# Kernel optimization log

Measured on AMD Instinct MI355X. Metric: run time of the kernel, lower is better.

Reference implementation:

```python
import jax, jax.numpy as jnp
import numpy as np

D = 1024        # model dim
H = 8           # num heads
HD = D // H     # head dim = 128
EPS = 1e-6
B, L = 2, 4096


def _rmsnorm(x, g):
    # RMSNorm over the full model dim (applied before head split, as in source)
    return x * jax.lax.rsqrt(jnp.mean(x * x, axis=-1, keepdims=True) + EPS) * g


def _rope_interleaved(x, cos, sin):
    # x: [B, L, H, HD]; cos/sin: [L, HD//2]
    x1 = x[..., 0::2]
    x2 = x[..., 1::2]
    c = cos[None, :, None, :]
    s = sin[None, :, None, :]
    # interleave (x1*c - x2*s, x1*s + x2*c) back into even/odd lanes
    out = jnp.stack([x1 * c - x2 * s, x1 * s + x2 * c], axis=-1)
    return out.reshape(x.shape)


def setup_inputs() -> dict:
    key = jax.random.key(0)
    ks = jax.random.split(key, 6)
    x = jax.random.normal(ks[0], (B, L, D), dtype=jnp.float32)
    freqs_cos = jax.random.uniform(ks[1], (L, HD // 2), dtype=jnp.float32)
    freqs_sin = jax.random.uniform(ks[2], (L, HD // 2), dtype=jnp.float32)
    s = 1.0 / np.sqrt(D).astype(np.float32)
    w_qkv = jax.random.normal(ks[3], (D, 3 * D), dtype=jnp.float32) * s
    b_qkv = jnp.zeros((3 * D,), dtype=jnp.float32)
    g_q = jnp.ones((D,), dtype=jnp.float32)
    g_k = jnp.ones((D,), dtype=jnp.float32)
    w_out = jax.random.normal(ks[4], (D, D), dtype=jnp.float32) * s
    b_out = jnp.zeros((D,), dtype=jnp.float32)
    return {"x": x, "freqs_cos": freqs_cos, "freqs_sin": freqs_sin,
            "w_qkv": w_qkv, "b_qkv": b_qkv, "g_q": g_q, "g_k": g_k,
            "w_out": w_out, "b_out": b_out}


def reference(x, freqs_cos, freqs_sin, w_qkv, b_qkv, g_q, g_k, w_out, b_out):
    Bx, Lx, _ = x.shape
    qkv = x @ w_qkv + b_qkv                      # [B, L, 3D]
    q, k, v = jnp.split(qkv, 3, axis=-1)          # each [B, L, D]
    q = _rmsnorm(q, g_q)
    k = _rmsnorm(k, g_k)
    q = q.reshape(Bx, Lx, H, HD)
    k = k.reshape(Bx, Lx, H, HD)
    v = v.reshape(Bx, Lx, H, HD)
    q = _rope_interleaved(q, freqs_cos, freqs_sin)
    k = _rope_interleaved(k, freqs_cos, freqs_sin)
    scale = 1.0 / np.sqrt(HD)
    scores = jnp.einsum('blhd,bmhd->bhlm', q, k) * scale
    attn = jax.nn.softmax(scores, axis=-1)
    o = jnp.einsum('bhlm,bmhd->blhd', attn, v).reshape(Bx, Lx, D)
    return o @ w_out + b_out
```

## Files before the change

kernel.cpp:

```cpp
#include <hip/hip_runtime.h>
#include <hip/hip_bf16.h>
#include <stdint.h>

typedef __attribute__((ext_vector_type(8))) short short8;
typedef __attribute__((ext_vector_type(4))) short short4v;
typedef __attribute__((ext_vector_type(4))) float f32x4;

#define LSEQ 4096
#define DMODEL 1024
#define NHEAD 8
#define HDIM 128
#define MTOT 8192
#define NQKV 3072

__device__ __forceinline__ unsigned short f2bf(float f){
  unsigned u = __float_as_uint(f);
  u += 0x7fffu + ((u >> 16) & 1u);
  return (unsigned short)(u >> 16);
}
__device__ __forceinline__ float bf2f(unsigned short h){
  return __uint_as_float(((unsigned)h) << 16);
}

typedef const __attribute__((address_space(1))) void* gas_ptr;
typedef __attribute__((address_space(3))) void* las_ptr;
__device__ __forceinline__ void gload_lds16(const void* g, void* l){
  __builtin_amdgcn_global_load_lds((gas_ptr)(uintptr_t)g,
                                   (las_ptr)(unsigned)(uintptr_t)l, 16, 0, 0);
}

__global__ __launch_bounds__(256) void k_cvt(const float* __restrict__ in,
                                             unsigned short* __restrict__ out, int n8){
  int i = blockIdx.x*256 + threadIdx.x;
  if (i >= n8) return;
  const float4* p = (const float4*)in + (size_t)i*2;
  float4 a = p[0], b = p[1];
  short8 r;
  r[0]=(short)f2bf(a.x); r[1]=(short)f2bf(a.y); r[2]=(short)f2bf(a.z); r[3]=(short)f2bf(a.w);
  r[4]=(short)f2bf(b.x); r[5]=(short)f2bf(b.y); r[6]=(short)f2bf(b.z); r[7]=(short)f2bf(b.w);
  *(short8*)(out + (size_t)i*8) = r;
}

__global__ __launch_bounds__(256) void k_transpose_cvt(const float* __restrict__ in,
                                                       unsigned short* __restrict__ out,
                                                       int R, int C){
  __shared__ unsigned short tile[32][33];
  int c0 = blockIdx.x*32, r0 = blockIdx.y*32;
  int tx = threadIdx.x & 31, ty = threadIdx.x >> 5;
  #pragma unroll
  for (int i=0;i<32;i+=8)
    tile[ty+i][tx] = f2bf(in[(size_t)(r0+ty+i)*C + c0+tx]);
  __syncthreads();
  #pragma unroll
  for (int i=0;i<32;i+=8)
    out[(size_t)(c0+ty+i)*R + r0+tx] = tile[tx][ty+i];
}

__global__ __launch_bounds__(256) void k_vT(const unsigned short* __restrict__ qkv,
                                            unsigned short* __restrict__ vT){
  __shared__ unsigned short tile[32][33];
  int bh = blockIdx.z; int b = bh >> 3, h = bh & 7;
  int l0 = blockIdx.x*32, d0 = blockIdx.y*32;
  const unsigned short* src = qkv + (size_t)b*LSEQ*NQKV + 2*DMODEL + h*HDIM;
  int tx = threadIdx.x & 31, ty = threadIdx.x >> 5;
  #pragma unroll
  for (int i=0;i<32;i+=8)
    tile[ty+i][tx] = src[(size_t)(l0+ty+i)*NQKV + d0+tx];
  __syncthreads();
  unsigned short* dst = vT + ((size_t)bh*HDIM + d0)*LSEQ + l0;
  #pragma unroll
  for (int i=0;i<32;i+=8)
    dst[(size_t)(ty+i)*LSEQ + tx] = tile[tx][ty+i];
}

template<int OUT_BF16>
__global__ __launch_bounds__(256) void k_gemm_bt(const unsigned short* __restrict__ A,
                                                 const unsigned short* __restrict__ Bt,
                                                 const float* __restrict__ bias,
                                                 void* __restrict__ Cout,
                                                 int M, int N, int K){
  __shared__ unsigned short As[128*64];
  __shared__ unsigned short Bs[128*64];
  int tid = threadIdx.x, lane = tid & 63, wave = tid >> 6;
  int wm = wave >> 1, wn = wave & 1;
  int m0 = blockIdx.y*128, n0 = blockIdx.x*128;
  f32x4 zero = {0.f,0.f,0.f,0.f};
  f32x4 acc[4][4];
  #pragma unroll
  for (int mi=0;mi<4;++mi)
    #pragma unroll
    for (int ni=0;ni<4;++ni) acc[mi][ni] = zero;

  int srow = lane >> 3;
  int soffb = (lane & 7) * 16;
  int scol = (soffb ^ (srow << 4)) >> 1;
  int cg = lane >> 4, cl = lane & 15;

  int nkt = K >> 6;
  for (int kt = 0; kt < nkt; ++kt){
    if (kt) __syncthreads();
    int kbase = kt*64;
    #pragma unroll
    for (int j=0;j<4;++j){
      int ch = wave*4 + j;
      int row = ch*8 + srow;
      gload_lds16(A  + (size_t)(m0+row)*K + kbase + scol, (char*)As + ch*1024);
      gload_lds16(Bt + (size_t)(n0+row)*K + kbase + scol, (char*)Bs + ch*1024);
    }
    __syncthreads();

    short8 af[4][2], bf[4][2];
    #pragma unroll
    for (int mi=0;mi<4;++mi){
      int row = wm*64 + mi*16 + cl;
      int key = (row & 7) << 4;
      #pragma unroll
      for (int kk=0;kk<2;++kk)
        af[mi][kk] = *(const short8*)((const char*)As + row*128 + ((kk*64 + cg*16) ^ key));
    }
    #pragma unroll
    for (int ni=0;ni<4;++ni){
      int row = wn*64 + ni*16 + cl;
      int key = (row & 7) << 4;
      #pragma unroll
      for (int kk=0;kk<2;++kk)
        bf[ni][kk] = *(const short8*)((const char*)Bs + row*128 + ((kk*64 + cg*16) ^ key));
    }
    #pragma unroll
    for (int kk=0;kk<2;++kk)
      #pragma unroll
      for (int mi=0;mi<4;++mi)
        #pragma unroll
        for (int ni=0;ni<4;++ni)
          acc[mi][ni] = __builtin_amdgcn_mfma_f32_16x16x32_bf16(af[mi][kk], bf[ni][kk], acc[mi][ni], 0,0,0);
  }

  #pragma unroll
  for (int ni=0;ni<4;++ni){
    int col = n0 + wn*64 + ni*16 + cl;
    float bv = bias[col];
    #pragma unroll
    for (int mi=0;mi<4;++mi){
      int r = m0 + wm*64 + mi*16 + cg*4;
      #pragma unroll
      for (int i=0;i<4;++i){
        float v = acc[mi][ni][i] + bv;
        if (OUT_BF16) ((unsigned short*)Cout)[(size_t)(r+i)*N + col] = f2bf(v);
        else          ((float*)Cout)[(size_t)(r+i)*N + col] = v;
      }
    }
  }
}

__global__ __launch_bounds__(256) void k_norm_rope(unsigned short* __restrict__ qkv,
                                                   const float* __restrict__ fcos,
                                                   const float* __restrict__ fsin,
                                                   const float* __restrict__ gq,
                                                   const float* __restrict__ gk){
  int bl = blockIdx.x;
  int l = bl & (LSEQ-1);
  int t = threadIdx.x;
  unsigned short* row = qkv + (size_t)bl * NQKV;
  int d0 = t*4;
  short4v qv = *(short4v*)(row + d0);
  short4v kv = *(short4v*)(row + DMODEL + d0);
  float q[4], k[4];
  #pragma unroll
  for (int j=0;j<4;++j){ q[j] = bf2f((unsigned short)qv[j]); k[j] = bf2f((unsigned short)kv[j]); }
  float sq = q[0]*q[0]+q[1]*q[1]+q[2]*q[2]+q[3]*q[3];
  float sk = k[0]*k[0]+k[1]*k[1]+k[2]*k[2]+k[3]*k[3];
  #pragma unroll
  for (int o=32;o;o>>=1){ sq += __shfl_xor(sq,o); sk += __shfl_xor(sk,o); }
  __shared__ float red[8];
  int lane = t & 63, wv = t >> 6;
  if (!lane){ red[wv] = sq; red[4+wv] = sk; }
  __syncthreads();
  sq = red[0]+red[1]+red[2]+red[3];
  sk = red[4]+red[5]+red[6]+red[7];
  float rq = rsqrtf(sq*(1.f/1024.f) + 1e-6f);
  float rk = rsqrtf(sk*(1.f/1024.f) + 1e-6f);
  int hd = d0 & (HDIM-1);
  int fi = (l << 6) + (hd >> 1);
  float c0 = fcos[fi], s0 = fsin[fi], c1 = fcos[fi+1], s1 = fsin[fi+1];
  {
    float x1 = q[0]*rq*gq[d0],   x2 = q[1]*rq*gq[d0+1];
    float x3 = q[2]*rq*gq[d0+2], x4 = q[3]*rq*gq[d0+3];
    short4v qo;
    qo[0]=(short)f2bf(x1*c0 - x2*s0); qo[1]=(short)f2bf(x1*s0 + x2*c0);
    qo[2]=(short)f2bf(x3*c1 - x4*s1); qo[3]=(short)f2bf(x3*s1 + x4*c1);
    *(short4v*)(row + d0) = qo;
  }
  {
    float x1 = k[0]*rk*gk[d0],   x2 = k[1]*rk*gk[d0+1];
    float x3 = k[2]*rk*gk[d0+2], x4 = k[3]*rk*gk[d0+3];
    short4v ko;
    ko[0]=(short)f2bf(x1*c0 - x2*s0); ko[1]=(short)f2bf(x1*s0 + x2*c0);
    ko[2]=(short)f2bf(x3*c1 - x4*s1); ko[3]=(short)f2bf(x3*s1 + x4*c1);
    *(short4v*)(row + DMODEL + d0) = ko;
  }
}

__global__ __launch_bounds__(256, 2) void k_attn(const unsigned short* __restrict__ qkv,
                                                 const unsigned short* __restrict__ vT,
                                                 unsigned short* __restrict__ o){
  __shared__ unsigned short Ks[2][64*128];
  __shared__ unsigned short VTs[2][128*64];
  __shared__ unsigned short Ps[4][2][16*64];
  int bh = blockIdx.y; int b = bh >> 3, h = bh & 7;
  int q0 = blockIdx.x * 128;
  int tid = threadIdx.x, lane = tid & 63, wave = tid >> 6;
  int cg = lane >> 4, cl = lane & 15;
  const unsigned short* base = qkv + (size_t)b*LSEQ*NQKV + h*HDIM;
  const unsigned short* kgl = base + DMODEL;
  const unsigned short* vtg = vT + (size_t)bh*HDIM*LSEQ;

  short8 qf[2][4];
  #pragma unroll
  for (int qs=0;qs<2;++qs){
    const unsigned short* qr = base + (size_t)(q0 + wave*32 + qs*16 + cl)*NQKV;
    #pragma unroll
    for (int kk=0;kk<4;++kk) qf[qs][kk] = *(const short8*)(qr + kk*32 + cg*8);
  }

  const float K2 = 0.12753568849800323f;
  float mrow[2] = {-3.0e38f, -3.0e38f}, lrow[2] = {0.f, 0.f};
  f32x4 zero = {0.f,0.f,0.f,0.f};
  f32x4 accO[2][8];
  #pragma unroll
  for (int qs=0;qs<2;++qs)
    #pragma unroll
    for (int dt=0;dt<8;++dt) accO[qs][dt] = zero;

  int keyc = (cl & 7) << 3;

  int k_row4 = cg;
  int v_dl   = lane >> 3;
  int v_srcb = ((lane & 7)*16) ^ (v_dl << 4);

  #pragma unroll
  for (int j=0;j<4;++j){
    int ch = wave*4 + j;
    int row = ch*4 + k_row4;
    int srcb = (cl*16) ^ ((row & 7) << 4);
    gload_lds16(kgl + (size_t)row*NQKV + (srcb >> 1), (char*)Ks[0] + ch*1024);
  }
  #pragma unroll
  for (int j=0;j<4;++j){
    int ch = wave*4 + j;
    int d = ch*8 + v_dl;
    gload_lds16(vtg + (size_t)d*LSEQ + (v_srcb >> 1), (char*)VTs[0] + ch*1024);
  }

  const int NT = LSEQ/64;
  for (int t = 0; t < NT; ++t){
    int cur = t & 1;
    __syncthreads();

    if (t+1 < NT){
      int kvn = (t+1)*64;
      #pragma unroll
      for (int j=0;j<4;++j){
        int ch = wave*4 + j;
        int row = ch*4 + k_row4;
        int srcb = (cl*16) ^ ((row & 7) << 4);
        gload_lds16(kgl + (size_t)(kvn+row)*NQKV + (srcb >> 1), (char*)Ks[cur^1] + ch*1024);
      }
      #pragma unroll
      for (int j=0;j<4;++j){
        int ch = wave*4 + j;
        int d = ch*8 + v_dl;
        gload_lds16(vtg + (size_t)d*LSEQ + kvn + (v_srcb >> 1), (char*)VTs[cur^1] + ch*1024);
      }
    }

    const char* kbuf = (const char*)Ks[cur];
    const unsigned short* vbuf = VTs[cur];

    f32x4 s[2][4];
    __builtin_amdgcn_s_setprio(1);
    #pragma unroll
    for (int nt=0;nt<4;++nt){
      f32x4 a0 = zero, a1 = zero;
      int rowb = (nt*16 + cl)*256;
      int key = (cl & 7) << 4;
      #pragma unroll
      for (int kkq=0;kkq<4;++kkq){
        short8 kf = *(const short8*)(kbuf + rowb + ((kkq*64 + cg*16) ^ key));
        a0 = __builtin_amdgcn_mfma_f32_16x16x32_bf16(kf, qf[0][kkq], a0, 0,0,0);
        a1 = __builtin_amdgcn_mfma_f32_16x16x32_bf16(kf, qf[1][kkq], a1, 0,0,0);
      }
      s[0][nt] = a0;
      s[1][nt] = a1;
    }
    __builtin_amdgcn_s_setprio(0);

    #pragma unroll
    for (int qs=0;qs<2;++qs){
      float mx = s[qs][0][0];
      #pragma unroll
      for (int nt=0;nt<4;++nt)
        #pragma unroll
        for (int i=0;i<4;++i) mx = fmaxf(mx, s[qs][nt][i]);
      mx = fmaxf(mx, __shfl_xor(mx, 16));
      mx = fmaxf(mx, __shfl_xor(mx, 32));
      float mx2 = mx * K2;
      bool rescale = !__all(mx2 <= mrow[qs] + 11.5416f);
      float fac = 1.f;
      if (rescale){
        float mn = fmaxf(mrow[qs], mx2);
        fac = exp2f(mrow[qs] - mn);
        mrow[qs] = mn;
      }
      float sum = 0.f;
      #pragma unroll
      for (int nt=0;nt<4;++nt)
        #pragma unroll
        for (int i=0;i<4;++i){
          float e = exp2f(fmaf(s[qs][nt][i], K2, -mrow[qs]));
          s[qs][nt][i] = e;
          sum += e;
        }
      lrow[qs] = lrow[qs]*fac + sum;
      if (rescale){
        float fq0 = __shfl(fac, (lane & 48) | (cg*4+0));
        float fq1 = __shfl(fac, (lane & 48) | (cg*4+1));
        float fq2 = __shfl(fac, (lane & 48) | (cg*4+2));
        float fq3 = __shfl(fac, (lane & 48) | (cg*4+3));
        #pragma unroll
        for (int dt=0;dt<8;++dt){
          f32x4 tv = accO[qs][dt];
          tv[0]*=fq0; tv[1]*=fq1; tv[2]*=fq2; tv[3]*=fq3;
          accO[qs][dt] = tv;
        }
      }
    }

    short8 pa0[2], pa1[2];
    #pragma unroll
    for (int qs=0;qs<2;++qs){
      unsigned short* pw = &Ps[wave][qs][0];
      #pragma unroll
      for (int nt=0;nt<4;++nt){
        unsigned p01, p23;
        asm("v_cvt_pk_bf16_f32 %0, %1, %2" : "=v"(p01) : "v"(s[qs][nt][0]), "v"(s[qs][nt][1]));
        asm("v_cvt_pk_bf16_f32 %0, %1, %2" : "=v"(p23) : "v"(s[qs][nt][2]), "v"(s[qs][nt][3]));
        uint2 pk; pk.x = p01; pk.y = p23;
        *(uint2*)&pw[cl*64 + ((nt*16 + cg*4) ^ keyc)] = pk;
      }
      pa0[qs] = *(const short8*)&pw[cl*64 + ((cg*8)      ^ keyc)];
      pa1[qs] = *(const short8*)&pw[cl*64 + ((32 + cg*8) ^ keyc)];
    }

    __builtin_amdgcn_s_setprio(1);
    #pragma unroll
    for (int dt=0;dt<8;++dt){
      const unsigned short* vrow = &vbuf[(dt*16 + cl)*64];
      short8 vf0 = *(const short8*)&vrow[(cg*8)      ^ keyc];
      short8 vf1 = *(const short8*)&vrow[(32 + cg*8) ^ keyc];
      accO[0][dt] = __builtin_amdgcn_mfma_f32_16x16x32_bf16(pa0[0], vf0, accO[0][dt], 0,0,0);
      accO[0][dt] = __builtin_amdgcn_mfma_f32_16x16x32_bf16(pa1[0], vf1, accO[0][dt], 0,0,0);
      accO[1][dt] = __builtin_amdgcn_mfma_f32_16x16x32_bf16(pa0[1], vf0, accO[1][dt], 0,0,0);
      accO[1][dt] = __builtin_amdgcn_mfma_f32_16x16x32_bf16(pa1[1], vf1, accO[1][dt], 0,0,0);
    }
    __builtin_amdgcn_s_setprio(0);
  }

  #pragma unroll
  for (int qs=0;qs<2;++qs){
    float lr = lrow[qs];
    lr += __shfl_xor(lr, 16);
    lr += __shfl_xor(lr, 32);
    float lq0 = __shfl(lr, (lane & 48) | (cg*4+0));
    float lq1 = __shfl(lr, (lane & 48) | (cg*4+1));
    float lq2 = __shfl(lr, (lane & 48) | (cg*4+2));
    float lq3 = __shfl(lr, (lane & 48) | (cg*4+3));
    float r0 = 1.f/lq0, r1 = 1.f/lq1, r2 = 1.f/lq2, r3 = 1.f/lq3;
    size_t orow = (size_t)(b*LSEQ + q0 + wave*32 + qs*16 + cg*4);
    #pragma unroll
    for (int dt=0;dt<8;++dt){
      int col = h*HDIM + dt*16 + cl;
      o[(orow+0)*DMODEL + col] = f2bf(accO[qs][dt][0]*r0);
      o[(orow+1)*DMODEL + col] = f2bf(accO[qs][dt][1]*r1);
      o[(orow+2)*DMODEL + col] = f2bf(accO[qs][dt][2]*r2);
      o[(orow+3)*DMODEL + col] = f2bf(accO[qs][dt][3]*r3);
    }
  }
}

extern "C" void kernel_launch(void* const* d_in, const int* in_sizes, int n_in,
                              void* d_out, int out_size, void* d_ws, size_t ws_size,
                              hipStream_t stream) {
  const float* x    = (const float*)d_in[0];
  const float* fcos = (const float*)d_in[1];
  const float* fsin = (const float*)d_in[2];
  const float* wqkv = (const float*)d_in[3];
  const float* bqkv = (const float*)d_in[4];
  const float* gq   = (const float*)d_in[5];
  const float* gk   = (const float*)d_in[6];
  const float* wout = (const float*)d_in[7];
  const float* bout = (const float*)d_in[8];
  float* out = (float*)d_out;

  char* ws = (char*)d_ws;
  unsigned short* xb    = (unsigned short*)(ws);
  unsigned short* qkv   = (unsigned short*)(ws + (16ull<<20));
  unsigned short* ob    = (unsigned short*)(ws + (64ull<<20));
  unsigned short* wqkvT = (unsigned short*)(ws + (80ull<<20));
  unsigned short* woutT = (unsigned short*)(ws + (86ull<<20));
  unsigned short* vT    = xb;

  k_cvt<<<4096, 256, 0, stream>>>(x, xb, (MTOT*DMODEL)/8);
  k_transpose_cvt<<<dim3(96,32), 256, 0, stream>>>(wqkv, wqkvT, DMODEL, NQKV);
  k_transpose_cvt<<<dim3(32,32), 256, 0, stream>>>(wout, woutT, DMODEL, DMODEL);
  k_gemm_bt<1><<<dim3(NQKV/128, MTOT/128), 256, 0, stream>>>(xb, wqkvT, bqkv, qkv, MTOT, NQKV, DMODEL);
  k_norm_rope<<<MTOT, 256, 0, stream>>>(qkv, fcos, fsin, gq, gk);
  k_vT<<<dim3(LSEQ/32, HDIM/32, 16), 256, 0, stream>>>(qkv, vT);
  k_attn<<<dim3(LSEQ/128, 16), 256, 0, stream>>>(qkv, vT, ob);
  k_gemm_bt<0><<<dim3(DMODEL/128, MTOT/128), 256, 0, stream>>>(ob, woutT, bout, out, MTOT, DMODEL, DMODEL);
}
```

Baseline: 323.1 us.

## Switch attention to 32x32x16 MFMA and pass P via permlane swap instead of LDS

Rewrites the flash-attention inner loop to use 32x32x16 bf16 MFMAs, with each wave handling 32 query rows as one tile. The scores are computed as S^T so the softmax row statistics sit in registers. The probability operand for the PV product is built in registers with v_permlane32_swap, which removes the per-wave LDS staging buffer, its stores and reloads. This aims to cut LDS traffic and per-MFMA overhead, at the cost of larger accumulator register footprints that may affect occupancy.

Measured after the change: 301.2 us. -6.8%, faster.

```diff
diff --git a/kernel.cpp b/kernel.cpp
--- a/kernel.cpp
+++ b/kernel.cpp
@@ -5,6 +5,7 @@
 typedef __attribute__((ext_vector_type(8))) short short8;
 typedef __attribute__((ext_vector_type(4))) short short4v;
 typedef __attribute__((ext_vector_type(4))) float f32x4;
+typedef __attribute__((ext_vector_type(16))) float f32x16;
 
 #define LSEQ 4096
 #define DMODEL 1024
@@ -205,43 +206,40 @@
                                                  unsigned short* __restrict__ o){
   __shared__ unsigned short Ks[2][64*128];
   __shared__ unsigned short VTs[2][128*64];
-  __shared__ unsigned short Ps[4][2][16*64];
   int bh = blockIdx.y; int b = bh >> 3, h = bh & 7;
   int q0 = blockIdx.x * 128;
   int tid = threadIdx.x, lane = tid & 63, wave = tid >> 6;
-  int cg = lane >> 4, cl = lane & 15;
+  int ql = lane & 31, hf = lane >> 5;
   const unsigned short* base = qkv + (size_t)b*LSEQ*NQKV + h*HDIM;
   const unsigned short* kgl = base + DMODEL;
   const unsigned short* vtg = vT + (size_t)bh*HDIM*LSEQ;
 
-  short8 qf[2][4];
-  #pragma unroll
-  for (int qs=0;qs<2;++qs){
-    const unsigned short* qr = base + (size_t)(q0 + wave*32 + qs*16 + cl)*NQKV;
-    #pragma unroll
-    for (int kk=0;kk<4;++kk) qf[qs][kk] = *(const short8*)(qr + kk*32 + cg*8);
+  short8 qf[8];
+  {
+    const unsigned short* qr = base + (size_t)(q0 + wave*32 + ql)*NQKV + hf*8;
+    #pragma unroll
+    for (int st=0;st<8;++st) qf[st] = *(const short8*)(qr + st*16);
   }
 
   const float K2 = 0.12753568849800323f;
-  float mrow[2] = {-3.0e38f, -3.0e38f}, lrow[2] = {0.f, 0.f};
-  f32x4 zero = {0.f,0.f,0.f,0.f};
-  f32x4 accO[2][8];
-  #pragma unroll
-  for (int qs=0;qs<2;++qs)
-    #pragma unroll
-    for (int dt=0;dt<8;++dt) accO[qs][dt] = zero;
-
-  int keyc = (cl & 7) << 3;
-
-  int k_row4 = cg;
+  float mrow = -3.0e38f, lrow = 0.f;
+  f32x16 z16 = {0.f};
+  f32x16 acc[4];
+  acc[0]=z16; acc[1]=z16; acc[2]=z16; acc[3]=z16;
+
+  int key = (ql & 7) << 4;
+
+  int k_row4 = lane >> 4;
+  (void)k_row4;
   int v_dl   = lane >> 3;
   int v_srcb = ((lane & 7)*16) ^ (v_dl << 4);
+  int cgk = (lane >> 4) & 3;
 
   #pragma unroll
   for (int j=0;j<4;++j){
     int ch = wave*4 + j;
-    int row = ch*4 + k_row4;
-    int srcb = (cl*16) ^ ((row & 7) << 4);
+    int row = ch*4 + cgk;
+    int srcb = ((lane & 15)*16) ^ ((row & 7) << 4);
     gload_lds16(kgl + (size_t)row*NQKV + (srcb >> 1), (char*)Ks[0] + ch*1024);
   }
   #pragma unroll
@@ -261,8 +259,8 @@
       #pragma unroll
       for (int j=0;j<4;++j){
         int ch = wave*4 + j;
-        int row = ch*4 + k_row4;
-        int srcb = (cl*16) ^ ((row & 7) << 4);
+        int row = ch*4 + cgk;
+        int srcb = ((lane & 15)*16) ^ ((row & 7) << 4);
         gload_lds16(kgl + (size_t)(kvn+row)*NQKV + (srcb >> 1), (char*)Ks[cur^1] + ch*1024);
       }
       #pragma unroll
@@ -273,116 +271,100 @@
       }
     }
 
-    const char* kbuf = (const char*)Ks[cur];
-    const unsigned short* vbuf = VTs[cur];
-
-    f32x4 s[2][4];
+    const char* kb = (const char*)Ks[cur];
+    const char* vb = (const char*)VTs[cur];
+
+    f32x16 s0 = z16, s1 = z16;
     __builtin_amdgcn_s_setprio(1);
     #pragma unroll
-    for (int nt=0;nt<4;++nt){
-      f32x4 a0 = zero, a1 = zero;
-      int rowb = (nt*16 + cl)*256;
-      int key = (cl & 7) << 4;
-      #pragma unroll
-      for (int kkq=0;kkq<4;++kkq){
-        short8 kf = *(const short8*)(kbuf + rowb + ((kkq*64 + cg*16) ^ key));
-        a0 = __builtin_amdgcn_mfma_f32_16x16x32_bf16(kf, qf[0][kkq], a0, 0,0,0);
-        a1 = __builtin_amdgcn_mfma_f32_16x16x32_bf16(kf, qf[1][kkq], a1, 0,0,0);
+    for (int st=0;st<8;++st){
+      int col = (hf*16 + st*32) ^ key;
+      short8 kf0 = *(const short8*)(kb + ql*256 + col);
+      short8 kf1 = *(const short8*)(kb + ql*256 + 8192 + col);
+      s0 = __builtin_amdgcn_mfma_f32_32x32x16_bf16(kf0, qf[st], s0, 0,0,0);
+      s1 = __builtin_amdgcn_mfma_f32_32x32x16_bf16(kf1, qf[st], s1, 0,0,0);
+    }
+    __builtin_amdgcn_s_setprio(0);
+
+    float mx = s0[0];
+    #pragma unroll
+    for (int i=1;i<16;++i) mx = fmaxf(mx, s0[i]);
+    #pragma unroll
+    for (int i=0;i<16;++i) mx = fmaxf(mx, s1[i]);
+    mx = fmaxf(mx, __shfl_xor(mx, 32));
+    float mx2 = mx * K2;
+    bool rescale = !__all(mx2 <= mrow + 11.5416f);
+    if (rescale){
+      float mn = fmaxf(mrow, mx2);
+      float fac = exp2f(mrow - mn);
+      mrow = mn;
+      lrow *= fac;
+      float fr[16];
+      #pragma unroll
+      for (int r=0;r<16;++r) fr[r] = __shfl(fac, (r&3) + 8*(r>>2) + 4*hf);
+      #pragma unroll
+      for (int dt=0;dt<4;++dt)
+        #pragma unroll
+        for (int r=0;r<16;++r) acc[dt][r] *= fr[r];
+    }
+    float sum = 0.f;
+    #pragma unroll
+    for (int i=0;i<16;++i){
+      float e = exp2f(fmaf(s0[i], K2, -mrow));
+      s0[i] = e; sum += e;
+    }
+    #pragma unroll
+    for (int i=0;i<16;++i){
+      float e = exp2f(fmaf(s1[i], K2, -mrow));
+      s1[i] = e; sum += e;
+    }
+    lrow += sum;
+
+    __builtin_amdgcn_s_setprio(1);
+    #pragma unroll
+    for (int c=0;c<4;++c){
+      unsigned c01, c23, c45, c67;
+      if (c < 2){
+        int rb = (c&1)*8;
+        asm("v_cvt_pk_bf16_f32 %0, %1, %2" : "=v"(c01) : "v"(s0[rb+0]), "v"(s0[rb+1]));
+        asm("v_cvt_pk_bf16_f32 %0, %1, %2" : "=v"(c23) : "v"(s0[rb+2]), "v"(s0[rb+3]));
+        asm("v_cvt_pk_bf16_f32 %0, %1, %2" : "=v"(c45) : "v"(s0[rb+4]), "v"(s0[rb+5]));
+        asm("v_cvt_pk_bf16_f32 %0, %1, %2" : "=v"(c67) : "v"(s0[rb+6]), "v"(s0[rb+7]));
+      } else {
+        int rb = (c&1)*8;
+        asm("v_cvt_pk_bf16_f32 %0, %1, %2" : "=v"(c01) : "v"(s1[rb+0]), "v"(s1[rb+1]));
+        asm("v_cvt_pk_bf16_f32 %0, %1, %2" : "=v"(c23) : "v"(s1[rb+2]), "v"(s1[rb+3]));
+        asm("v_cvt_pk_bf16_f32 %0, %1, %2" : "=v"(c45) : "v"(s1[rb+4]), "v"(s1[rb+5]));
+        asm("v_cvt_pk_bf16_f32 %0, %1, %2" : "=v"(c67) : "v"(s1[rb+6]), "v"(s1[rb+7]));
       }
-      s[0][nt] = a0;
-      s[1][nt] = a1;
+      asm("v_permlane32_swap_b32 %0, %1" : "+v"(c01), "+v"(c45));
+      asm("v_permlane32_swap_b32 %0, %1" : "+v"(c23), "+v"(c67));
+      union { unsigned u[4]; short8 v; } pu;
+      pu.u[0] = c01; pu.u[1] = c23; pu.u[2] = c45; pu.u[3] = c67;
+      short8 pa = pu.v;
+      #pragma unroll
+      for (int dt=0;dt<4;++dt){
+        int col = (c*32 + hf*16) ^ key;
+        short8 vf = *(const short8*)(vb + (dt*32 + ql)*128 + col);
+        acc[dt] = __builtin_amdgcn_mfma_f32_32x32x16_bf16(pa, vf, acc[dt], 0,0,0);
+      }
     }
     __builtin_amdgcn_s_setprio(0);
-
-    #pragma unroll
-    for (int qs=0;qs<2;++qs){
-      float mx = s[qs][0][0];
-      #pragma unroll
-      for (int nt=0;nt<4;++nt)
-        #pragma unroll
-        for (int i=0;i<4;++i) mx = fmaxf(mx, s[qs][nt][i]);
-      mx = fmaxf(mx, __shfl_xor(mx, 16));
-      mx = fmaxf(mx, __shfl_xor(mx, 32));
-      float mx2 = mx * K2;
-      bool rescale = !__all(mx2 <= mrow[qs] + 11.5416f);
-      float fac = 1.f;
-      if (rescale){
-        float mn = fmaxf(mrow[qs], mx2);
-        fac = exp2f(mrow[qs] - mn);
-        mrow[qs] = mn;
-      }
-      float sum = 0.f;
-      #pragma unroll
-      for (int nt=0;nt<4;++nt)
-        #pragma unroll
-        for (int i=0;i<4;++i){
-          float e = exp2f(fmaf(s[qs][nt][i], K2, -mrow[qs]));
-          s[qs][nt][i] = e;
-          sum += e;
-        }
-      lrow[qs] = lrow[qs]*fac + sum;
-      if (rescale){
-        float fq0 = __shfl(fac, (lane & 48) | (cg*4+0));
-        float fq1 = __shfl(fac, (lane & 48) | (cg*4+1));
-        float fq2 = __shfl(fac, (lane & 48) | (cg*4+2));
-        float fq3 = __shfl(fac, (lane & 48) | (cg*4+3));
-        #pragma unroll
-        for (int dt=0;dt<8;++dt){
-          f32x4 tv = accO[qs][dt];
-          tv[0]*=fq0; tv[1]*=fq1; tv[2]*=fq2; tv[3]*=fq3;
-          accO[qs][dt] = tv;
-        }
-      }
-    }
-
-    short8 pa0[2], pa1[2];
-    #pragma unroll
-    for (int qs=0;qs<2;++qs){
-      unsigned short* pw = &Ps[wave][qs][0];
-      #pragma unroll
-      for (int nt=0;nt<4;++nt){
-        unsigned p01, p23;
-        asm("v_cvt_pk_bf16_f32 %0, %1, %2" : "=v"(p01) : "v"(s[qs][nt][0]), "v"(s[qs][nt][1]));
-        asm("v_cvt_pk_bf16_f32 %0, %1, %2" : "=v"(p23) : "v"(s[qs][nt][2]), "v"(s[qs][nt][3]));
-        uint2 pk; pk.x = p01; pk.y = p23;
-        *(uint2*)&pw[cl*64 + ((nt*16 + cg*4) ^ keyc)] = pk;
-      }
-      pa0[qs] = *(const short8*)&pw[cl*64 + ((cg*8)      ^ keyc)];
-      pa1[qs] = *(const short8*)&pw[cl*64 + ((32 + cg*8) ^ keyc)];
-    }
-
-    __builtin_amdgcn_s_setprio(1);
-    #pragma unroll
-    for (int dt=0;dt<8;++dt){
-      const unsigned short* vrow = &vbuf[(dt*16 + cl)*64];
-      short8 vf0 = *(const short8*)&vrow[(cg*8)      ^ keyc];
-      short8 vf1 = *(const short8*)&vrow[(32 + cg*8) ^ keyc];
-      accO[0][dt] = __builtin_amdgcn_mfma_f32_16x16x32_bf16(pa0[0], vf0, accO[0][dt], 0,0,0);
-      accO[0][dt] = __builtin_amdgcn_mfma_f32_16x16x32_bf16(pa1[0], vf1, accO[0][dt], 0,0,0);
-      accO[1][dt] = __builtin_amdgcn_mfma_f32_16x16x32_bf16(pa0[1], vf0, accO[1][dt], 0,0,0);
-      accO[1][dt] = __builtin_amdgcn_mfma_f32_16x16x32_bf16(pa1[1], vf1, accO[1][dt], 0,0,0);
-    }
-    __builtin_amdgcn_s_setprio(0);
-  }
-
-  #pragma unroll
-  for (int qs=0;qs<2;++qs){
-    float lr = lrow[qs];
-    lr += __shfl_xor(lr, 16);
-    lr += __shfl_xor(lr, 32);
-    float lq0 = __shfl(lr, (lane & 48) | (cg*4+0));
-    float lq1 = __shfl(lr, (lane & 48) | (cg*4+1));
-    float lq2 = __shfl(lr, (lane & 48) | (cg*4+2));
-    float lq3 = __shfl(lr, (lane & 48) | (cg*4+3));
-    float r0 = 1.f/lq0, r1 = 1.f/lq1, r2 = 1.f/lq2, r3 = 1.f/lq3;
-    size_t orow = (size_t)(b*LSEQ + q0 + wave*32 + qs*16 + cg*4);
-    #pragma unroll
-    for (int dt=0;dt<8;++dt){
-      int col = h*HDIM + dt*16 + cl;
-      o[(orow+0)*DMODEL + col] = f2bf(accO[qs][dt][0]*r0);
-      o[(orow+1)*DMODEL + col] = f2bf(accO[qs][dt][1]*r1);
-      o[(orow+2)*DMODEL + col] = f2bf(accO[qs][dt][2]*r2);
-      o[(orow+3)*DMODEL + col] = f2bf(accO[qs][dt][3]*r3);
+  }
+
+  lrow += __shfl_xor(lrow, 32);
+  float rl = 1.f / lrow;
+  float rr[16];
+  #pragma unroll
+  for (int r=0;r<16;++r) rr[r] = __shfl(rl, (r&3) + 8*(r>>2) + 4*hf);
+  size_t qbase = (size_t)(b*LSEQ + q0 + wave*32);
+  #pragma unroll
+  for (int dt=0;dt<4;++dt){
+    int col = h*HDIM + dt*32 + ql;
+    #pragma unroll
+    for (int r=0;r<16;++r){
+      int qrow = (r&3) + 8*(r>>2) + 4*hf;
+      o[(qbase + qrow)*DMODEL + col] = f2bf(acc[dt][r]*rr[r]);
     }
   }
 }
```
